# Kernel tuning notes

Hardware: AMD Instinct MI355X
Metric: run time of the kernel (lower is better)

## Reference

```python
import jax, jax.numpy as jnp
import numpy as np

D_MODEL = 1024
NUM_HEADS = 16
D_K = D_MODEL // NUM_HEADS
THETA = 10000.0
BATCH = 4
SEQ = 2048


def rope(x, positions, theta=THETA):
    # x: [B, H, S, d_k]; rotate interleaved pairs (x_{2i}, x_{2i+1})
    d_k = x.shape[-1]
    inv_freq = theta ** (-jnp.arange(0, d_k, 2, dtype=jnp.float32) / d_k)  # [d_k/2]
    ang = positions[:, None].astype(jnp.float32) * inv_freq[None, :]  # [S, d_k/2]
    cos, sin = jnp.cos(ang), jnp.sin(ang)
    x1 = x[..., 0::2]
    x2 = x[..., 1::2]
    r1 = x1 * cos - x2 * sin
    r2 = x1 * sin + x2 * cos
    out = jnp.stack([r1, r2], axis=-1).reshape(x.shape)
    return out.astype(x.dtype)


def setup_inputs() -> dict:
    key = jax.random.key(0)
    k0, k1, k2, k3, k4 = jax.random.split(key, 5)
    std_qk = 2.0 / (D_MODEL + D_MODEL)
    x = jax.random.normal(k0, (BATCH, SEQ, D_MODEL), dtype=jnp.float32)
    P_Q = jax.random.normal(k1, (D_MODEL, D_MODEL), dtype=jnp.float32) * std_qk
    P_K = jax.random.normal(k2, (D_MODEL, D_MODEL), dtype=jnp.float32) * std_qk
    P_V = jax.random.normal(k3, (D_MODEL, D_MODEL), dtype=jnp.float32) * std_qk
    P_O = jax.random.normal(k4, (D_MODEL, D_MODEL), dtype=jnp.float32) * std_qk
    return {"x": x, "P_Q": P_Q, "P_K": P_K, "P_V": P_V, "P_O": P_O}


def reference(x, P_Q, P_K, P_V, P_O):
    B, S, _ = x.shape
    positions = jnp.arange(S)

    def proj(P):
        y = jnp.einsum('bsd,ed->bse', x, P)  # e = num_heads*d_k
        return y.reshape(B, S, NUM_HEADS, D_K).transpose(0, 2, 1, 3)  # [B,H,S,d_k]

    Q = rope(proj(P_Q), positions)
    K = rope(proj(P_K), positions)
    V = proj(P_V)

    scores = jnp.einsum('bhqd,bhkd->bhqk', Q, K) / jnp.sqrt(jnp.asarray(D_K, x.dtype))
    causal = jnp.tril(jnp.ones((S, S), dtype=bool))
    scores = jnp.where(causal, scores, jnp.asarray(-jnp.inf, scores.dtype))
    attn = jax.nn.softmax(scores, axis=-1)
    out = jnp.einsum('bhqk,bhkd->bhqd', attn, V)  # [B,H,S,d_v]
    out = out.transpose(0, 2, 1, 3).reshape(B, S, NUM_HEADS * D_K)
    return jnp.einsum('bse,de->bsd', out, P_O)
```

## Files before the change

### kernel.cpp

```cpp
#include <hip/hip_runtime.h>

typedef unsigned short u16;
typedef unsigned int u32;
typedef float f32x4 __attribute__((ext_vector_type(4)));
typedef __bf16 bf16x8 __attribute__((ext_vector_type(8)));

#define S_LEN 2048
#define DMODEL 1024
#define NHEAD 16
#define DKH 64

__device__ __forceinline__ u16 f2bf(float f) {
    unsigned u = __float_as_uint(f);
    u += 0x7FFFu + ((u >> 16) & 1u);
    return (u16)(u >> 16);
}

__device__ __forceinline__ u32 pkbf2(float a, float b) {
#if __has_builtin(__builtin_amdgcn_cvt_pk_bf16_f32)
    typedef __bf16 bf16x2_t __attribute__((ext_vector_type(2)));
    bf16x2_t r = __builtin_amdgcn_cvt_pk_bf16_f32(a, b);
    u32 u; __builtin_memcpy(&u, &r, 4); return u;
#else
    return (u32)f2bf(a) | ((u32)f2bf(b) << 16);
#endif
}

#if __has_builtin(__builtin_amdgcn_exp2f)
#define EXP2(x) __builtin_amdgcn_exp2f(x)
#else
#define EXP2(x) exp2f(x)
#endif

__device__ __forceinline__ void lds_fence_wave() {
    __asm__ volatile("" ::: "memory");
    __builtin_amdgcn_s_waitcnt(0xC07F);
    __asm__ volatile("" ::: "memory");
}

__device__ __forceinline__ void glds16(const u16* g, u16* l) {
    __builtin_amdgcn_global_load_lds(
        (const __attribute__((address_space(1))) void*)(g),
        (__attribute__((address_space(3))) void*)(l), 16, 0, 0);
}

__global__ __launch_bounds__(256) void cvt_all(const float* __restrict__ x, const float* __restrict__ PQ,
                                               const float* __restrict__ PK, const float* __restrict__ PV,
                                               const float* __restrict__ PO,
                                               u16* __restrict__ xb, u16* __restrict__ Wqkv,
                                               u16* __restrict__ Wo) {
    int i = blockIdx.x * 256 + threadIdx.x;
    const float* src; u16* dst; int j;
    if (i < 2097152)      { src = x;  dst = xb;             j = i; }
    else if (i < 2359296) { src = PQ; dst = Wqkv;           j = i - 2097152; }
    else if (i < 2621440) { src = PK; dst = Wqkv + 1048576; j = i - 2359296; }
    else if (i < 2883584) { src = PV; dst = Wqkv + 2097152; j = i - 2621440; }
    else                  { src = PO; dst = Wo;             j = i - 2883584; }
    float4 v = reinterpret_cast<const float4*>(src)[j];
    uint2 o;
    o.x = pkbf2(v.x, v.y);
    o.y = pkbf2(v.z, v.w);
    reinterpret_cast<uint2*>(dst)[j] = o;
}

__device__ __forceinline__ void gemm_core(const u16* __restrict__ A, const u16* __restrict__ Bt,
                                          int K, int m0, int n0,
                                          u16* As, u16* Bs, f32x4 acc[4][4]) {
    const int tid  = threadIdx.x;
    const int lane = tid & 63;
    const int quad = lane >> 4, l15 = lane & 15;
    const int w    = tid >> 6;
    const int mq   = w & 1, nq = w >> 1;

    const int c0 = tid, c1 = tid + 256;
    const int r0 = c0 >> 2, k0 = ((c0 & 3) ^ (r0 & 3)) * 8;
    const int r1 = c1 >> 2, k1 = ((c1 & 3) ^ (r1 & 3)) * 8;
    const u16* ga0 = A  + (size_t)(m0 + r0) * K + k0;
    const u16* ga1 = A  + (size_t)(m0 + r1) * K + k1;
    const u16* gb0 = Bt + (size_t)(n0 + r0) * K + k0;
    const u16* gb1 = Bt + (size_t)(n0 + r1) * K + k1;
    u16* la0 = As + c0 * 8; u16* la1 = As + c1 * 8;
    u16* lb0 = Bs + c0 * 8; u16* lb1 = Bs + c1 * 8;

    const int swz = (quad ^ (l15 & 3)) * 8;
    const u16* ra = As + (mq * 64 + l15) * 32 + swz;
    const u16* rb = Bs + (nq * 64 + l15) * 32 + swz;

    for (int kk = 0; kk < K; kk += 32) {
        __syncthreads();
        glds16(ga0 + kk, la0);
        glds16(ga1 + kk, la1);
        glds16(gb0 + kk, lb0);
        glds16(gb1 + kk, lb1);
        __syncthreads();
        bf16x8 af[4], bfv[4];
#pragma unroll
        for (int t = 0; t < 4; ++t) {
            af[t]  = *reinterpret_cast<const bf16x8*>(ra + t * 512);
            bfv[t] = *reinterpret_cast<const bf16x8*>(rb + t * 512);
        }
#pragma unroll
        for (int mt = 0; mt < 4; ++mt)
#pragma unroll
            for (int nt = 0; nt < 4; ++nt)
                acc[mt][nt] = __builtin_amdgcn_mfma_f32_16x16x32_bf16(af[mt], bfv[nt], acc[mt][nt], 0, 0, 0);
    }
}

__global__ __launch_bounds__(256) void gemm_qkv_kernel(const u16* __restrict__ xb, const u16* __restrict__ Wqkv,
                                                       u16* __restrict__ Qb, u16* __restrict__ Kb,
                                                       u16* __restrict__ Vt) {
    __shared__ u16 As[128 * 32];
    __shared__ u16 Bs[128 * 32];
    f32x4 acc[4][4];
    const f32x4 zz = {0.f, 0.f, 0.f, 0.f};
#pragma unroll
    for (int i = 0; i < 4; ++i)
#pragma unroll
        for (int j = 0; j < 4; ++j) acc[i][j] = zz;

    const int m0 = blockIdx.y * 128;
    const int n0 = blockIdx.x * 128;
    gemm_core(xb, Wqkv, DMODEL, m0, n0, As, Bs, acc);

    const int lane = threadIdx.x & 63;
    const int quad = lane >> 4, l15 = lane & 15;
    const int w = threadIdx.x >> 6, mq = w & 1, nq = w >> 1;

#pragma unroll
    for (int nt = 0; nt < 4; ++nt) {
        const int ncol = n0 + nq*64 + nt*16 + l15;
        const int sel  = ncol >> 10;
        const int e    = ncol & 1023;
        const int h    = e >> 6, dk = e & 63;
#pragma unroll
        for (int mt = 0; mt < 4; ++mt) {
            const int mrow = m0 + mq*64 + mt*16 + quad*4;
            if (sel == 2) {
                int b = mrow >> 11, s = mrow & 2047;
                uint2 pv;
                pv.x = pkbf2(acc[mt][nt][0], acc[mt][nt][1]);
                pv.y = pkbf2(acc[mt][nt][2], acc[mt][nt][3]);
                *reinterpret_cast<uint2*>(&Vt[((size_t)(b * NHEAD + h) * DKH + dk) * S_LEN + s]) = pv;
            } else {
                float invf_rev = 0.15915494f * exp2f(-13.2877124f * (float)(dk & 62) * (1.0f / 64.0f));
                const float sc = sel ? 1.0f : 0.18033688f;
                u16* dst = sel ? Kb : Qb;
#pragma unroll
                for (int r = 0; r < 4; ++r) {
                    float val  = acc[mt][nt][r];
                    float part = __shfl_xor(val, 1);
                    int m = mrow + r;
                    int b = m >> 11, s = m & 2047;
                    float rev = (float)s * invf_rev;
                    float fr  = rev - floorf(rev);
#if __has_builtin(__builtin_amdgcn_sinf) && __has_builtin(__builtin_amdgcn_cosf)
                    float sn = __builtin_amdgcn_sinf(fr);
                    float cs = __builtin_amdgcn_cosf(fr);
#else
                    float sn, cs;
                    __sincosf(fr * 6.2831853f, &sn, &cs);
#endif
                    sn *= sc; cs *= sc;
                    float o = (dk & 1) ? (part * sn + val * cs)
                                       : (val * cs - part * sn);
                    dst[((size_t)(b * NHEAD + h) * S_LEN + s) * DKH + dk] = f2bf(o);
                }
            }
        }
    }
}

__global__ __launch_bounds__(256) void attn_kernel(const u16* __restrict__ Qb, const u16* __restrict__ Kb,
                                                   const u16* __restrict__ Vt, u16* __restrict__ A2) {
    __shared__ u16 Ks[2][64 * 64];
    __shared__ u16 Vs[2][64 * 64];
    __shared__ u16 Ps[4][32 * 64];

    const int tid  = threadIdx.x;
    const int lane = tid & 63, w = tid >> 6;
    const int quad = lane >> 4, l15 = lane & 15;
    const int bh   = blockIdx.x & 63;
    const int qb   = 15 - (blockIdx.x >> 6);
    const int b = bh >> 4, h = bh & 15;
    const int q0w = qb * 128 + w * 32;
    const int nkt = 2 * (qb + 1);
    const int sw7 = l15 & 7;
    const f32x4 zz = {0.f, 0.f, 0.f, 0.f};

    uint4 ob; ob.x = ob.y = ob.z = ob.w = 0x3F803F80u;
    bf16x8 ones; __builtin_memcpy(&ones, &ob, 16);

    bf16x8 qf[2][2];
#pragma unroll
    for (int qt2 = 0; qt2 < 2; ++qt2)
#pragma unroll
        for (int hh = 0; hh < 2; ++hh)
            qf[qt2][hh] = *reinterpret_cast<const bf16x8*>(
                Qb + ((size_t)bh * S_LEN + q0w + qt2 * 16 + l15) * DKH + hh * 32 + quad * 8);

    f32x4 ot[4][2], lacc[2];
#pragma unroll
    for (int mt = 0; mt < 4; ++mt) { ot[mt][0] = zz; ot[mt][1] = zz; }
    lacc[0] = zz; lacc[1] = zz;

    const int c0 = tid, c1 = tid + 256;
    const int r0 = c0 >> 3, kc0 = ((c0 & 7) ^ (r0 & 7)) * 8;
    const int r1 = c1 >> 3, kc1 = ((c1 & 7) ^ (r1 & 7)) * 8;
    const u16* gk0 = Kb + ((size_t)bh * S_LEN + r0) * DKH + kc0;
    const u16* gk1 = Kb + ((size_t)bh * S_LEN + r1) * DKH + kc1;
    const u16* gv0 = Vt + ((size_t)bh * DKH + r0) * S_LEN + kc0;
    const u16* gv1 = Vt + ((size_t)bh * DKH + r1) * S_LEN + kc1;
    u16* Pw = &Ps[w][0];
    u16* prow0 = Pw + l15 * 64 + (quad & 1) * 4;
    u16* prow1 = Pw + (16 + l15) * 64 + (quad & 1) * 4;

    auto stage = [&](u16* kdst, u16* vdst, int kt) {
        const size_t key0 = (size_t)kt * 64;
        glds16(gk0 + key0 * DKH, kdst + c0 * 8);
        glds16(gk1 + key0 * DKH, kdst + c1 * 8);
        glds16(gv0 + key0,       vdst + c0 * 8);
        glds16(gv1 + key0,       vdst + c1 * 8);
    };

    auto compute = [&](const u16* Kbuf, const u16* Vbuf, int key0) {
        f32x4 st[4][2];
#pragma unroll
        for (int kt4 = 0; kt4 < 4; ++kt4) {
            const u16* krow = Kbuf + (kt4 * 16 + l15) * 64;
            bf16x8 ka0 = *reinterpret_cast<const bf16x8*>(krow + (quad ^ sw7) * 8);
            bf16x8 ka1 = *reinterpret_cast<const bf16x8*>(krow + ((4 + quad) ^ sw7) * 8);
#pragma unroll
            for (int qt2 = 0; qt2 < 2; ++qt2) {
                f32x4 s = __builtin_amdgcn_mfma_f32_16x16x32_bf16(ka0, qf[qt2][0], zz, 0, 0, 0);
                st[kt4][qt2] = __builtin_amdgcn_mfma_f32_16x16x32_bf16(ka1, qf[qt2][1], s, 0, 0, 0);
            }
        }
        if (key0 + 63 > q0w) {
#pragma unroll
            for (int qt2 = 0; qt2 < 2; ++qt2) {
                const int qrow = q0w + qt2 * 16 + l15;
#pragma unroll
                for (int kt4 = 0; kt4 < 4; ++kt4) {
                    const int kbase = key0 + kt4 * 16 + quad * 4;
#pragma unroll
                    for (int r = 0; r < 4; ++r)
                        if (kbase + r > qrow) st[kt4][qt2][r] = -3.0e38f;
                }
            }
        }
#pragma unroll
        for (int qt2 = 0; qt2 < 2; ++qt2) {
            u16* prow = qt2 ? prow1 : prow0;
#pragma unroll
            for (int kt4 = 0; kt4 < 4; ++kt4) {
                uint2 pv;
                pv.x = pkbf2(EXP2(st[kt4][qt2][0]), EXP2(st[kt4][qt2][1]));
                pv.y = pkbf2(EXP2(st[kt4][qt2][2]), EXP2(st[kt4][qt2][3]));
                *reinterpret_cast<uint2*>(prow + ((2 * kt4 + (quad >> 1)) ^ sw7) * 8) = pv;
            }
        }
        lds_fence_wave();
        bf16x8 pb[2][2];
#pragma unroll
        for (int qt2 = 0; qt2 < 2; ++qt2)
#pragma unroll
            for (int kh = 0; kh < 2; ++kh)
                pb[qt2][kh] = *reinterpret_cast<const bf16x8*>(
                    Pw + (qt2 * 16 + l15) * 64 + ((kh * 4 + quad) ^ sw7) * 8);
#pragma unroll
        for (int mt = 0; mt < 4; ++mt) {
            const u16* vrow = Vbuf + (mt * 16 + l15) * 64;
            bf16x8 va0 = *reinterpret_cast<const bf16x8*>(vrow + (quad ^ sw7) * 8);
            bf16x8 va1 = *reinterpret_cast<const bf16x8*>(vrow + ((4 + quad) ^ sw7) * 8);
#pragma unroll
            for (int qt2 = 0; qt2 < 2; ++qt2) {
                ot[mt][qt2] = __builtin_amdgcn_mfma_f32_16x16x32_bf16(va0, pb[qt2][0], ot[mt][qt2], 0, 0, 0);
                ot[mt][qt2] = __builtin_amdgcn_mfma_f32_16x16x32_bf16(va1, pb[qt2][1], ot[mt][qt2], 0, 0, 0);
            }
        }
#pragma unroll
        for (int qt2 = 0; qt2 < 2; ++qt2) {
            lacc[qt2] = __builtin_amdgcn_mfma_f32_16x16x32_bf16(ones, pb[qt2][0], lacc[qt2], 0, 0, 0);
            lacc[qt2] = __builtin_amdgcn_mfma_f32_16x16x32_bf16(ones, pb[qt2][1], lacc[qt2], 0, 0, 0);
        }
    };

    stage(&Ks[0][0], &Vs[0][0], 0);
#pragma unroll 1
    for (int kt = 0; kt < nkt; kt += 2) {
        __syncthreads();
        stage(&Ks[1][0], &Vs[1][0], kt + 1);
        compute(&Ks[0][0], &Vs[0][0], kt * 64);
        __syncthreads();
        if (kt + 2 < nkt) stage(&Ks[0][0], &Vs[0][0], kt + 2);
        compute(&Ks[1][0], &Vs[1][0], (kt + 1) * 64);
    }

    lds_fence_wave();
#pragma unroll
    for (int qt2 = 0; qt2 < 2; ++qt2) {
        const float il = 1.0f / lacc[qt2][0];
        u16* prow = qt2 ? prow1 : prow0;
#pragma unroll
        for (int mt = 0; mt < 4; ++mt) {
            uint2 ov;
            ov.x = pkbf2(ot[mt][qt2][0] * il, ot[mt][qt2][1] * il);
            ov.y = pkbf2(ot[mt][qt2][2] * il, ot[mt][qt2][3] * il);
            *reinterpret_cast<uint2*>(prow + ((2 * mt + (quad >> 1)) ^ sw7) * 8) = ov;
        }
    }
    lds_fence_wave();
    const int r2 = lane >> 1, half = lane & 1;
    const u16* orow = Pw + r2 * 64;
    u16* gout = A2 + ((size_t)b * S_LEN + q0w + r2) * DMODEL + h * DKH + half * 32;
#pragma unroll
    for (int c = 0; c < 4; ++c) {
        uint4 val = *reinterpret_cast<const uint4*>(orow + (((half * 4 + c) ^ (r2 & 7))) * 8);
        *reinterpret_cast<uint4*>(gout + c * 8) = val;
    }
}

__global__ __launch_bounds__(256) void gemm_oproj_kernel(const u16* __restrict__ A2, const u16* __restrict__ Wo,
                                                         float* __restrict__ Cout) {
    __shared__ u16 As[128 * 32];
    __shared__ u16 Bs[128 * 32];
    f32x4 acc[4][4];
    const f32x4 zz = {0.f, 0.f, 0.f, 0.f};
#pragma unroll
    for (int i = 0; i < 4; ++i)
#pragma unroll
        for (int j = 0; j < 4; ++j) acc[i][j] = zz;

    const int m0 = blockIdx.y * 128;
    const int n0 = blockIdx.x * 128;
    gemm_core(A2, Wo, DMODEL, m0, n0, As, Bs, acc);

    const int lane = threadIdx.x & 63;
    const int quad = lane >> 4, l15 = lane & 15;
    const int w = threadIdx.x >> 6, mq = w & 1, nq = w >> 1;
#pragma unroll
    for (int nt = 0; nt < 4; ++nt) {
        const int ncol = n0 + nq*64 + nt*16 + l15;
#pragma unroll
        for (int mt = 0; mt < 4; ++mt) {
            const int mrow = m0 + mq*64 + mt*16 + quad*4;
#pragma unroll
            for (int r = 0; r < 4; ++r)
                Cout[(size_t)(mrow + r) * DMODEL + ncol] = acc[mt][nt][r];
        }
    }
}

extern "C" void kernel_launch(void* const* d_in, const int* in_sizes, int n_in,
                              void* d_out, int out_size, void* d_ws, size_t ws_size,
                              hipStream_t stream) {
    const float* x  = (const float*)d_in[0];
    const float* PQ = (const float*)d_in[1];
    const float* PK = (const float*)d_in[2];
    const float* PV = (const float*)d_in[3];
    const float* PO = (const float*)d_in[4];
    float* out = (float*)d_out;
    char* ws = (char*)d_ws;

    const size_t MB = 1u << 20;
    u16* xb   = (u16*)(ws + 0 * MB);
    u16* Wqkv = (u16*)(ws + 16 * MB);
    u16* Wo   = (u16*)(ws + 22 * MB);
    u16* Qb   = (u16*)(ws + 24 * MB);
    u16* Kb   = (u16*)(ws + 40 * MB);
    u16* Vt   = (u16*)(ws + 56 * MB);
    u16* A2   = (u16*)(ws + 72 * MB);

    cvt_all<<<dim3(12288), dim3(256), 0, stream>>>(x, PQ, PK, PV, PO, xb, Wqkv, Wo);

    gemm_qkv_kernel<<<dim3(24, 64), dim3(256), 0, stream>>>(xb, Wqkv, Qb, Kb, Vt);

    attn_kernel<<<dim3(1024), dim3(256), 0, stream>>>(Qb, Kb, Vt, A2);

    gemm_oproj_kernel<<<dim3(8, 64), dim3(256), 0, stream>>>(A2, Wo, out);
}
```

Measured before the change: 272.4 us.

## Double-buffer LDS tiles in GEMM core and change swizzle pattern

The shared GEMM core now keeps two LDS stages for the A and B tiles. It issues the global-to-LDS copy for the next K-step before running MFMAs on the current one, and needs only one barrier per iteration instead of two. The XOR swizzle now keys on row pairs rather than single rows, aimed at reducing LDS bank conflicts on the 16-byte fragment reads. This doubles the LDS footprint of the QKV and output-projection GEMM kernels, which may lower occupancy. The RoPE frequency computation also switches from exp2f to an EXP2 macro.

```diff
diff --git a/kernel.cpp b/kernel.cpp
--- a/kernel.cpp
+++ b/kernel.cpp
@@ -73,26 +73,31 @@
     const int mq   = w & 1, nq = w >> 1;
 
     const int c0 = tid, c1 = tid + 256;
-    const int r0 = c0 >> 2, k0 = ((c0 & 3) ^ (r0 & 3)) * 8;
-    const int r1 = c1 >> 2, k1 = ((c1 & 3) ^ (r1 & 3)) * 8;
+    const int r0 = c0 >> 2, k0 = ((c0 & 3) ^ ((r0 >> 1) & 3)) * 8;
+    const int r1 = c1 >> 2, k1 = ((c1 & 3) ^ ((r1 >> 1) & 3)) * 8;
     const u16* ga0 = A  + (size_t)(m0 + r0) * K + k0;
     const u16* ga1 = A  + (size_t)(m0 + r1) * K + k1;
     const u16* gb0 = Bt + (size_t)(n0 + r0) * K + k0;
     const u16* gb1 = Bt + (size_t)(n0 + r1) * K + k1;
-    u16* la0 = As + c0 * 8; u16* la1 = As + c1 * 8;
-    u16* lb0 = Bs + c0 * 8; u16* lb1 = Bs + c1 * 8;
-
-    const int swz = (quad ^ (l15 & 3)) * 8;
-    const u16* ra = As + (mq * 64 + l15) * 32 + swz;
-    const u16* rb = Bs + (nq * 64 + l15) * 32 + swz;
-
+
+    const int swz = (quad ^ ((l15 >> 1) & 3)) * 8;
+
+    auto stage = [&](int buf, int kk) {
+        u16* ad = As + buf * 4096;
+        u16* bd = Bs + buf * 4096;
+        glds16(ga0 + kk, ad + c0 * 8);
+        glds16(ga1 + kk, ad + c1 * 8);
+        glds16(gb0 + kk, bd + c0 * 8);
+        glds16(gb1 + kk, bd + c1 * 8);
+    };
+
+    stage(0, 0);
     for (int kk = 0; kk < K; kk += 32) {
+        const int cur = (kk >> 5) & 1;
         __syncthreads();
-        glds16(ga0 + kk, la0);
-        glds16(ga1 + kk, la1);
-        glds16(gb0 + kk, lb0);
-        glds16(gb1 + kk, lb1);
-        __syncthreads();
+        if (kk + 32 < K) stage(cur ^ 1, kk + 32);
+        const u16* ra = As + cur * 4096 + (mq * 64 + l15) * 32 + swz;
+        const u16* rb = Bs + cur * 4096 + (nq * 64 + l15) * 32 + swz;
         bf16x8 af[4], bfv[4];
 #pragma unroll
         for (int t = 0; t < 4; ++t) {
@@ -110,8 +115,8 @@
 __global__ __launch_bounds__(256) void gemm_qkv_kernel(const u16* __restrict__ xb, const u16* __restrict__ Wqkv,
                                                        u16* __restrict__ Qb, u16* __restrict__ Kb,
                                                        u16* __restrict__ Vt) {
-    __shared__ u16 As[128 * 32];
-    __shared__ u16 Bs[128 * 32];
+    __shared__ u16 As[2 * 128 * 32];
+    __shared__ u16 Bs[2 * 128 * 32];
     f32x4 acc[4][4];
     const f32x4 zz = {0.f, 0.f, 0.f, 0.f};
 #pragma unroll
@@ -143,7 +148,7 @@
                 pv.y = pkbf2(acc[mt][nt][2], acc[mt][nt][3]);
                 *reinterpret_cast<uint2*>(&Vt[((size_t)(b * NHEAD + h) * DKH + dk) * S_LEN + s]) = pv;
             } else {
-                float invf_rev = 0.15915494f * exp2f(-13.2877124f * (float)(dk & 62) * (1.0f / 64.0f));
+                float invf_rev = 0.15915494f * EXP2(-13.2877124f * (float)(dk & 62) * (1.0f / 64.0f));
                 const float sc = sel ? 1.0f : 0.18033688f;
                 u16* dst = sel ? Kb : Qb;
 #pragma unroll
@@ -323,8 +328,8 @@
 
 __global__ __launch_bounds__(256) void gemm_oproj_kernel(const u16* __restrict__ A2, const u16* __restrict__ Wo,
                                                          float* __restrict__ Cout) {
-    __shared__ u16 As[128 * 32];
-    __shared__ u16 Bs[128 * 32];
+    __shared__ u16 As[2 * 128 * 32];
+    __shared__ u16 Bs[2 * 128 * 32];
     f32x4 acc[4][4];
     const f32x4 zz = {0.f, 0.f, 0.f, 0.f};
 #pragma unroll
```

Result: faster. 258.9 us (-5.0%).
